# Performance work log

Hardware: AMD Instinct MI355X
Metric: run time of the kernel (lower is better)

Reference implementation:

```python
import jax, jax.numpy as jnp
import numpy as np

N_SRC = 100000
N_DST = 100000
N_EDGES = 300000
FEAT = 256
REV_DIM = 128
REV_VOCAB = 500000


def setup_inputs() -> dict:
    key = jax.random.key(0)
    ks = jax.random.split(key, 14)
    feat = jax.random.normal(ks[0], (N_SRC, FEAT), dtype=jnp.float32)
    cj = jax.random.uniform(ks[1], (N_SRC, 1), dtype=jnp.float32)
    ci = jax.random.uniform(ks[2], (N_DST, 1), dtype=jnp.float32)
    edge_src = jax.random.randint(ks[3], (N_EDGES,), 0, N_SRC)
    edge_dst = jax.random.randint(ks[4], (N_EDGES,), 0, N_DST)
    review_id = jax.random.randint(ks[5], (N_EDGES,), 0, REV_VOCAB)
    s = 0.05
    review_emb = jax.random.normal(ks[6], (REV_VOCAB, REV_DIM), dtype=jnp.float32) * s
    prob_w = jax.random.normal(ks[7], (1, REV_DIM), dtype=jnp.float32) * s      # prob_score
    score_w = jax.random.normal(ks[8], (1, REV_DIM), dtype=jnp.float32) * s     # review_score
    rw1 = jax.random.normal(ks[9], (FEAT, REV_DIM), dtype=jnp.float32) * s      # review_w[0]
    rw2 = jax.random.normal(ks[10], (FEAT, FEAT), dtype=jnp.float32) * s        # review_w[2]
    rw3 = jax.random.normal(ks[11], (FEAT, FEAT), dtype=jnp.float32) * s        # review_w[4]
    lin_w = jax.random.normal(ks[12], (FEAT, FEAT), dtype=jnp.float32) * s      # self.linear
    lin_b = jax.random.normal(ks[13], (FEAT,), dtype=jnp.float32) * s
    return dict(feat=feat, cj=cj, ci=ci, edge_src=edge_src, edge_dst=edge_dst,
                review_id=review_id, review_emb=review_emb, prob_w=prob_w,
                score_w=score_w, rw1=rw1, rw2=rw2, rw3=rw3, lin_w=lin_w, lin_b=lin_b)


def reference(feat, cj, ci, edge_src, edge_dst, review_id,
              review_emb, prob_w, score_w, rw1, rw2, rw3, lin_w, lin_b):
    gelu = lambda x: jax.nn.gelu(x, approximate=False)  # torch default GELU (erf)
    # gather review embeddings per edge: [E, 128]
    rfeat = review_emb[review_id]
    pa = jax.nn.sigmoid(rfeat @ prob_w.T)    # [E, 1]
    ra = jax.nn.sigmoid(rfeat @ score_w.T)   # [E, 1]
    # review_w MLP: 128 -> F -> F -> F, no bias, GELU between
    rf = gelu(gelu(rfeat @ rw1.T) @ rw2.T) @ rw3.T  # [E, F]
    # per-edge message, gated and normalized by src cj (dropout is identity at p=0)
    m = (feat[edge_src] * pa + rf * ra) * cj[edge_src]  # [E, F]
    # scatter-sum to destination nodes
    h = jax.ops.segment_sum(m, edge_dst, num_segments=N_DST)  # [N_dst, F]
    rst = h * ci
    return rst @ lin_w.T + lin_b
```

## Files before the change

### kernel.cpp

```cpp
#include <hip/hip_runtime.h>
#include <math.h>
#include <stdint.h>


typedef short bf16x8 __attribute__((ext_vector_type(8)));
typedef float f32x16 __attribute__((ext_vector_type(16)));

__device__ __forceinline__ float bf2f(unsigned short v) {
    union { unsigned int u; float f; } x; x.u = ((unsigned int)v) << 16; return x.f;
}
__device__ __forceinline__ unsigned short f2bf(float f) {
    union { float f; unsigned int u; } x; x.f = f;
    unsigned int u = x.u;
    return (unsigned short)((u + 0x7FFFu + ((u >> 16) & 1u)) >> 16);
}
__device__ __forceinline__ unsigned pack2(float lo, float hi) {
    unsigned r;
    asm("v_cvt_pk_bf16_f32 %0, %1, %2" : "=v"(r) : "v"(lo), "v"(hi));
    return r;
}
__device__ __forceinline__ float gelu_fast(float x) {
    float y = x * (0.7978845608f + 0.0356774081f * x * x);
    float e = __builtin_amdgcn_exp2f(y * 2.8853900818f);
    float th = 1.0f - 2.0f * __builtin_amdgcn_rcpf(e + 1.0f);
    return 0.5f * x * (1.0f + th);
}
__device__ __forceinline__ float sigmoidf(float x) {
    return 1.0f / (1.0f + expf(-x));
}

__global__ __launch_bounds__(256) void prep_weights(
    const float* __restrict__ rw1, const float* __restrict__ rw2,
    const float* __restrict__ rw3, const float* __restrict__ lw,
    unsigned short* __restrict__ w1s, unsigned short* __restrict__ w2s,
    unsigned short* __restrict__ w3s, unsigned short* __restrict__ lws)
{
    int i = blockIdx.x * blockDim.x + threadIdx.x;
    int j   = i & 7;
    int l   = (i >> 3) & 31;
    int kgg = (i >> 8) & 1;
    int n2  = (i >> 9) & 7;
    int ks  = i >> 12;
    if (i < 32768) {
        w1s[i] = f2bf(rw1[(n2 * 32 + l) * 128 + ks * 16 + kgg * 8 + j]);
    }
    if (i < 65536) {
        int row = n2 * 32 + l, k = ks * 16 + kgg * 8 + j;
        w2s[i] = f2bf(rw2[(size_t)row * 256 + k]);
        w3s[i] = f2bf(rw3[(size_t)row * 256 + k]);
        int ok = (k & 192) | ((k & 1) << 5) | ((k & 63) >> 1);
        lws[i] = f2bf(lw[(size_t)row * 256 + ok]);
    }
}

__device__ __forceinline__ bf16x8 ldw(const unsigned short* __restrict__ W,
                                      int ks, int nglob, int kg, int l31) {
    return *(const bf16x8*)(W + (((((ks * 8 + nglob) * 2) + kg) * 32 + l31) << 3));
}

__global__ __launch_bounds__(256) void hist_kernel(
    const int* __restrict__ edst, int* __restrict__ cnt,
    int* __restrict__ within, int E)
{
    int e = blockIdx.x * blockDim.x + threadIdx.x;
    if (e < E) within[e] = atomicAdd(&cnt[edst[e]], 1);
}

__global__ __launch_bounds__(1024) void scan_block(
    const int* __restrict__ cnt, int* __restrict__ start,
    int* __restrict__ bsum, int n)
{
    __shared__ int s[1024];
    int gid = blockIdx.x * 1024 + threadIdx.x;
    int v = (gid < n) ? cnt[gid] : 0;
    s[threadIdx.x] = v;
    __syncthreads();
    #pragma unroll
    for (int off = 1; off < 1024; off <<= 1) {
        int t = (threadIdx.x >= off) ? s[threadIdx.x - off] : 0;
        __syncthreads();
        if (threadIdx.x >= off) s[threadIdx.x] += t;
        __syncthreads();
    }
    if (gid < n) start[gid] = s[threadIdx.x] - v;
    if (threadIdx.x == 1023) bsum[blockIdx.x] = s[1023];
}

__global__ void scan_bsum(int* __restrict__ bsum, int nb) {
    if (threadIdx.x == 0 && blockIdx.x == 0) {
        int acc = 0;
        for (int i = 0; i < nb; ++i) { int v = bsum[i]; bsum[i] = acc; acc += v; }
    }
}

__global__ __launch_bounds__(1024) void add_offsets(
    int* __restrict__ start, const int* __restrict__ bsum, int n, int E)
{
    int gid = blockIdx.x * 1024 + threadIdx.x;
    if (gid < n) start[gid] += bsum[gid >> 10];
    if (gid == 0) start[n] = E;
}

__global__ __launch_bounds__(256) void build_sorted(
    const int* __restrict__ edst, const int* __restrict__ within,
    const int* __restrict__ start, const int* __restrict__ rid,
    const int* __restrict__ esrc, int* __restrict__ rid_s,
    int* __restrict__ esrc_s, int E)
{
    int e = blockIdx.x * blockDim.x + threadIdx.x;
    if (e < E) {
        int pos = start[edst[e]] + within[e];
        rid_s[pos]  = rid[e];
        esrc_s[pos] = esrc[e];
    }
}

__device__ __forceinline__ bf16x8 ldtf(const unsigned short* t_lds, int row, int ks, int kg) {
    int slot = (ks * 2 + kg) ^ (row & 15);
    return *(const bf16x8*)((const char*)t_lds + row * 512 + slot * 16);
}
__device__ __forceinline__ void sttf(unsigned short* t_lds, int row, int nn, int p, int kg, uint2 w) {
    int slot = (nn * 4 + p) ^ (row & 15);
    *(uint2*)((char*)t_lds + row * 512 + slot * 16 + kg * 8) = w;
}
__device__ __forceinline__ bf16x8 ldrb(const unsigned short* t_rb, int row, int ks, int kg) {
    int slot = (ks * 2 + kg) ^ (row & 15);
    return *(const bf16x8*)((const char*)t_rb + row * 256 + slot * 16);
}

__global__ __launch_bounds__(256, 5) void fused_edge(
    const float* __restrict__ remb, const int* __restrict__ rid_s,
    const int* __restrict__ esrc_s,
    const unsigned short* __restrict__ w1s, const unsigned short* __restrict__ w2s,
    const unsigned short* __restrict__ w3s,
    const float* __restrict__ pw, const float* __restrict__ sw,
    const float* __restrict__ cj, float* __restrict__ ga,
    unsigned short* __restrict__ m, int E)
{
    __shared__ __align__(16) unsigned short t_lds[32 * 256];
    __shared__ __align__(16) unsigned short t_rb[32 * 128];
    __shared__ float gvb_lds[32];

    const int lane = threadIdx.x & 63;
    const int f    = threadIdx.x >> 6;
    const int l31  = lane & 31;
    const int kg   = lane >> 5;
    const int blk0 = blockIdx.x * 32;
    const int i    = blk0 + l31;
    const int ic   = (i < E) ? i : (E - 1);
    const int row_l = l31;

    {
        const int t = threadIdx.x;
        #pragma unroll
        for (int p = 0; p < 2; ++p) {
            int sIdx = p * 256 + t;
            int row  = sIdx >> 4;
            int c16  = sIdx & 15;
            int gr   = blk0 + row;
            int rr   = rid_s[(gr < E) ? gr : (E - 1)];
            const float* sp = remb + (size_t)rr * 128 + c16 * 8;
            float4 a = *(const float4*)sp;
            float4 b = *(const float4*)(sp + 4);
            uint4 w;
            w.x = pack2(a.x, a.y); w.y = pack2(a.z, a.w);
            w.z = pack2(b.x, b.y); w.w = pack2(b.z, b.w);
            int slot = c16 ^ (row & 15);
            *(uint4*)((char*)t_rb + row * 256 + slot * 16) = w;
        }
    }
    __syncthreads();

    {
        f32x16 acc[2];
        acc[0] = (f32x16)0.0f; acc[1] = (f32x16)0.0f;
        float pd = 0.f, rd = 0.f;

        #pragma unroll
        for (int ks = 0; ks < 8; ++ks) {
            bf16x8 af = ldrb(t_rb, row_l, ks, kg);
            if (f == 0) {
                const int kk = ks * 16 + kg * 8;
                float4 p0 = *(const float4*)(pw + kk), p1 = *(const float4*)(pw + kk + 4);
                float4 s0 = *(const float4*)(sw + kk), s1v = *(const float4*)(sw + kk + 4);
                float v0 = bf2f((unsigned short)af[0]), v1 = bf2f((unsigned short)af[1]);
                float v2 = bf2f((unsigned short)af[2]), v3 = bf2f((unsigned short)af[3]);
                float v4 = bf2f((unsigned short)af[4]), v5 = bf2f((unsigned short)af[5]);
                float v6 = bf2f((unsigned short)af[6]), v7 = bf2f((unsigned short)af[7]);
                pd += v0*p0.x + v1*p0.y + v2*p0.z + v3*p0.w
                    + v4*p1.x + v5*p1.y + v6*p1.z + v7*p1.w;
                rd += v0*s0.x + v1*s0.y + v2*s0.z + v3*s0.w
                    + v4*s1v.x + v5*s1v.y + v6*s1v.z + v7*s1v.w;
            }
            #pragma unroll
            for (int n = 0; n < 2; ++n) {
                bf16x8 wf = ldw(w1s, ks, f * 2 + n, kg, l31);
                acc[n] = __builtin_amdgcn_mfma_f32_32x32x16_bf16(wf, af, acc[n], 0, 0, 0);
            }
        }

        if (f == 0) {
            pd += __shfl_xor(pd, 32);
            rd += __shfl_xor(rd, 32);
            if (lane < 32) {
                float cjv = cj[esrc_s[ic]];
                if (i < E) ga[i] = sigmoidf(pd) * cjv;
                gvb_lds[l31] = sigmoidf(rd) * cjv;
            }
        }

        #pragma unroll
        for (int n = 0; n < 2; ++n)
            #pragma unroll
            for (int p = 0; p < 4; ++p) {
                uint2 w;
                w.x = pack2(gelu_fast(acc[n][4*p + 0]), gelu_fast(acc[n][4*p + 1]));
                w.y = pack2(gelu_fast(acc[n][4*p + 2]), gelu_fast(acc[n][4*p + 3]));
                sttf(t_lds, row_l, f * 2 + n, p, kg, w);
            }
    }
    __syncthreads();

    {
        f32x16 acc[2];
        acc[0] = (f32x16)0.0f; acc[1] = (f32x16)0.0f;

        #pragma unroll
        for (int ks = 0; ks < 16; ++ks) {
            bf16x8 tf = ldtf(t_lds, row_l, ks, kg);
            #pragma unroll
            for (int n = 0; n < 2; ++n) {
                bf16x8 wf = ldw(w2s, ks, f * 2 + n, kg, l31);
                acc[n] = __builtin_amdgcn_mfma_f32_32x32x16_bf16(wf, tf, acc[n], 0, 0, 0);
            }
        }
        __syncthreads();
        #pragma unroll
        for (int n = 0; n < 2; ++n)
            #pragma unroll
            for (int p = 0; p < 4; ++p) {
                uint2 w;
                w.x = pack2(gelu_fast(acc[n][4*p + 0]), gelu_fast(acc[n][4*p + 1]));
                w.y = pack2(gelu_fast(acc[n][4*p + 2]), gelu_fast(acc[n][4*p + 3]));
                sttf(t_lds, row_l, f * 2 + n, p, kg, w);
            }
    }
    __syncthreads();

    {
        f32x16 acc[2];
        acc[0] = (f32x16)0.0f; acc[1] = (f32x16)0.0f;

        #pragma unroll
        for (int ks = 0; ks < 16; ++ks) {
            bf16x8 tf = ldtf(t_lds, row_l, ks, kg);
            #pragma unroll
            for (int n = 0; n < 2; ++n) {
                bf16x8 wf = ldw(w3s, ks, f * 2 + n, kg, l31);
                acc[n] = __builtin_amdgcn_mfma_f32_32x32x16_bf16(tf, wf, acc[n], 0, 0, 0);
            }
        }

        #pragma unroll
        for (int r = 0; r < 16; ++r) {
            const int lrow = (r & 3) + 8 * (r >> 2) + 4 * kg;
            const int gi = blk0 + lrow;
            if (gi < E) {
                float gbv = gvb_lds[lrow];
                float v0 = acc[0][r] * gbv;
                float v1 = acc[1][r] * gbv;
                *(unsigned*)(m + (size_t)gi * 256 + f * 64 + l31 * 2) = pack2(v0, v1);
            }
        }
    }
}

__global__ __launch_bounds__(256) void segsum_kernel(
    const int* __restrict__ start, const unsigned short* __restrict__ m,
    const float* __restrict__ ga, const int* __restrict__ esrc_s,
    const float* __restrict__ feat, unsigned short* __restrict__ h, int ND)
{
    int d = blockIdx.x * 4 + (threadIdx.x >> 6);
    if (d >= ND) return;
    int lane = threadIdx.x & 63;
    int q = lane >> 4;
    int b = lane & 15;
    int foff = q * 64 + 2 * b;
    int s0 = start[d], s1 = start[d + 1];
    float a0 = 0.f, a1 = 0.f, a2 = 0.f, a3 = 0.f;
    for (int i = s0; i < s1; ++i) {
        float gav = ga[i];
        const float* fp = feat + (size_t)esrc_s[i] * 256 + foff;
        float2 fa = *(const float2*)fp;
        float2 fb = *(const float2*)(fp + 32);
        ushort4 v = *(const ushort4*)(m + (size_t)i * 256 + lane * 4);
        a0 += bf2f(v.x) + fa.x * gav;
        a1 += bf2f(v.y) + fb.x * gav;
        a2 += bf2f(v.z) + fa.y * gav;
        a3 += bf2f(v.w) + fb.y * gav;
    }
    ushort4 o; o.x = f2bf(a0); o.y = f2bf(a1); o.z = f2bf(a2); o.w = f2bf(a3);
    *(ushort4*)(h + (size_t)d * 256 + lane * 4) = o;
}

__global__ __launch_bounds__(256, 2) void g4_kernel(
    const unsigned short* __restrict__ Ab, const unsigned short* __restrict__ lws,
    float* __restrict__ outf, const float* __restrict__ ci,
    const float* __restrict__ bias, int M)
{
    const int lane = threadIdx.x & 63;
    const int wid  = threadIdx.x >> 6;
    const int l31  = lane & 31;
    const int kg   = lane >> 5;
    const int f    = wid & 1;
    const int wbase = blockIdx.x * 128 + (wid >> 1) * 64;
    const int r0 = wbase + l31, r1 = wbase + 32 + l31;
    const int ar0 = (r0 < M) ? r0 : (M - 1);
    const int ar1 = (r1 < M) ? r1 : (M - 1);

    f32x16 acc[2][4];
    #pragma unroll
    for (int mi = 0; mi < 2; ++mi)
        #pragma unroll
        for (int n = 0; n < 4; ++n) acc[mi][n] = (f32x16)0.0f;

    #pragma unroll
    for (int ks = 0; ks < 16; ++ks) {
        const int kk = ks * 16 + kg * 8;
        bf16x8 a0 = *(const bf16x8*)(Ab + (size_t)ar0 * 256 + kk);
        bf16x8 a1 = *(const bf16x8*)(Ab + (size_t)ar1 * 256 + kk);
        #pragma unroll
        for (int n = 0; n < 4; ++n) {
            bf16x8 b = ldw(lws, ks, f * 4 + n, kg, l31);
            acc[0][n] = __builtin_amdgcn_mfma_f32_32x32x16_bf16(a0, b, acc[0][n], 0, 0, 0);
            acc[1][n] = __builtin_amdgcn_mfma_f32_32x32x16_bf16(a1, b, acc[1][n], 0, 0, 0);
        }
    }
    #pragma unroll
    for (int mi = 0; mi < 2; ++mi) {
        #pragma unroll
        for (int r = 0; r < 16; ++r) {
            const int gr = wbase + mi * 32 + (r & 3) + 8 * (r >> 2) + 4 * kg;
            if (gr >= M) continue;
            float civ = ci[gr];
            #pragma unroll
            for (int n = 0; n < 4; ++n) {
                int col = f * 128 + n * 32 + l31;
                outf[(size_t)gr * 256 + col] = acc[mi][n][r] * civ + bias[col];
            }
        }
    }
}

extern "C" void kernel_launch(void* const* d_in, const int* in_sizes, int n_in,
                              void* d_out, int out_size, void* d_ws, size_t ws_size,
                              hipStream_t stream) {
    const float* feat = (const float*)d_in[0];
    const float* cj   = (const float*)d_in[1];
    const float* ci   = (const float*)d_in[2];
    const int*   esrc = (const int*)d_in[3];
    const int*   edst = (const int*)d_in[4];
    const int*   rid  = (const int*)d_in[5];
    const float* remb = (const float*)d_in[6];
    const float* pw   = (const float*)d_in[7];
    const float* sw   = (const float*)d_in[8];
    const float* rw1  = (const float*)d_in[9];
    const float* rw2  = (const float*)d_in[10];
    const float* rw3  = (const float*)d_in[11];
    const float* lw   = (const float*)d_in[12];
    const float* lb   = (const float*)d_in[13];
    float* out = (float*)d_out;

    const int E  = in_sizes[3];
    const int ND = in_sizes[2];

    char* ws = (char*)d_ws;
    float* ga = (float*)ws;
    unsigned short* m   = (unsigned short*)(ga + E);
    unsigned short* h   = m + (size_t)E * 256;
    unsigned short* w1s = h + (size_t)ND * 256;
    unsigned short* w2s = w1s + 32768;
    unsigned short* w3s = w2s + 65536;
    unsigned short* lws = w3s + 65536;
    int* cnt    = (int*)(lws + 65536);
    int* start  = cnt + ND;
    int* bsum   = start + ND + 1;
    int* within = bsum + 128;
    int* rid_s  = within + E;
    int* esrc_s = rid_s + E;

    const int NB = (ND + 1023) / 1024;

    hipMemsetAsync(cnt, 0, (size_t)ND * sizeof(int), stream);
    prep_weights<<<256, 256, 0, stream>>>(rw1, rw2, rw3, lw, w1s, w2s, w3s, lws);

    hist_kernel<<<(E + 255) / 256, 256, 0, stream>>>(edst, cnt, within, E);
    scan_block<<<NB, 1024, 0, stream>>>(cnt, start, bsum, ND);
    scan_bsum<<<1, 64, 0, stream>>>(bsum, NB);
    add_offsets<<<NB, 1024, 0, stream>>>(start, bsum, ND, E);
    build_sorted<<<(E + 255) / 256, 256, 0, stream>>>(edst, within, start, rid, esrc,
                                                      rid_s, esrc_s, E);

    fused_edge<<<(E + 31) / 32, 256, 0, stream>>>(
        remb, rid_s, esrc_s, w1s, w2s, w3s, pw, sw, cj, ga, m, E);

    segsum_kernel<<<(ND + 3) / 4, 256, 0, stream>>>(start, m, ga, esrc_s, feat, h, ND);

    g4_kernel<<<(ND + 127) / 128, 256, 0, stream>>>(h, lws, out, ci, lb, ND);
}
```

Measured before the change: 418.9 us.

## Fuse segment-sum into edge MLP kernel and drop per-edge message buffer

```diff
diff --git a/kernel.cpp b/kernel.cpp
--- a/kernel.cpp
+++ b/kernel.cpp
@@ -48,8 +48,7 @@
         int row = n2 * 32 + l, k = ks * 16 + kgg * 8 + j;
         w2s[i] = f2bf(rw2[(size_t)row * 256 + k]);
         w3s[i] = f2bf(rw3[(size_t)row * 256 + k]);
-        int ok = (k & 192) | ((k & 1) << 5) | ((k & 63) >> 1);
-        lws[i] = f2bf(lw[(size_t)row * 256 + ok]);
+        lws[i] = f2bf(lw[(size_t)row * 256 + k]);
     }
 }
 
@@ -105,13 +104,15 @@
     const int* __restrict__ edst, const int* __restrict__ within,
     const int* __restrict__ start, const int* __restrict__ rid,
     const int* __restrict__ esrc, int* __restrict__ rid_s,
-    int* __restrict__ esrc_s, int E)
+    int* __restrict__ esrc_s, int* __restrict__ dst_s, int E)
 {
     int e = blockIdx.x * blockDim.x + threadIdx.x;
     if (e < E) {
-        int pos = start[edst[e]] + within[e];
+        int d = edst[e];
+        int pos = start[d] + within[e];
         rid_s[pos]  = rid[e];
         esrc_s[pos] = esrc[e];
+        dst_s[pos]  = d;
     }
 }
 
@@ -130,28 +131,36 @@
 
 __global__ __launch_bounds__(256, 5) void fused_edge(
     const float* __restrict__ remb, const int* __restrict__ rid_s,
-    const int* __restrict__ esrc_s,
+    const int* __restrict__ esrc_s, const int* __restrict__ dst_s,
+    const int* __restrict__ start,
     const unsigned short* __restrict__ w1s, const unsigned short* __restrict__ w2s,
     const unsigned short* __restrict__ w3s,
     const float* __restrict__ pw, const float* __restrict__ sw,
-    const float* __restrict__ cj, float* __restrict__ ga,
-    unsigned short* __restrict__ m, int E)
+    const float* __restrict__ cj, const float* __restrict__ feat,
+    unsigned short* __restrict__ h, int E)
 {
     __shared__ __align__(16) unsigned short t_lds[32 * 256];
     __shared__ __align__(16) unsigned short t_rb[32 * 128];
-    __shared__ float gvb_lds[32];
+    __shared__ float ga_lds[32], gvb_lds[32];
+    __shared__ int dst_lds[32], src_lds[32], cross_lds[32];
 
     const int lane = threadIdx.x & 63;
     const int f    = threadIdx.x >> 6;
     const int l31  = lane & 31;
     const int kg   = lane >> 5;
     const int blk0 = blockIdx.x * 32;
-    const int i    = blk0 + l31;
-    const int ic   = (i < E) ? i : (E - 1);
     const int row_l = l31;
 
     {
         const int t = threadIdx.x;
+        if (t < 32) {
+            int e  = blk0 + t;
+            int ec = (e < E) ? e : (E - 1);
+            int d  = dst_s[ec];
+            dst_lds[t]   = d;
+            src_lds[t]   = esrc_s[ec];
+            cross_lds[t] = (start[d] < blk0) || (start[d + 1] > blk0 + 32);
+        }
         #pragma unroll
         for (int p = 0; p < 2; ++p) {
             int sIdx = p * 256 + t;
@@ -203,8 +212,8 @@
             pd += __shfl_xor(pd, 32);
             rd += __shfl_xor(rd, 32);
             if (lane < 32) {
-                float cjv = cj[esrc_s[ic]];
-                if (i < E) ga[i] = sigmoidf(pd) * cjv;
+                float cjv = cj[src_lds[l31]];
+                ga_lds[l31]  = sigmoidf(pd) * cjv;
                 gvb_lds[l31] = sigmoidf(rd) * cjv;
             }
         }
@@ -262,45 +271,37 @@
         }
 
         #pragma unroll
-        for (int r = 0; r < 16; ++r) {
-            const int lrow = (r & 3) + 8 * (r >> 2) + 4 * kg;
-            const int gi = blk0 + lrow;
-            if (gi < E) {
-                float gbv = gvb_lds[lrow];
-                float v0 = acc[0][r] * gbv;
-                float v1 = acc[1][r] * gbv;
-                *(unsigned*)(m + (size_t)gi * 256 + f * 64 + l31 * 2) = pack2(v0, v1);
-            }
-        }
-    }
-}
-
-__global__ __launch_bounds__(256) void segsum_kernel(
-    const int* __restrict__ start, const unsigned short* __restrict__ m,
-    const float* __restrict__ ga, const int* __restrict__ esrc_s,
-    const float* __restrict__ feat, unsigned short* __restrict__ h, int ND)
-{
-    int d = blockIdx.x * 4 + (threadIdx.x >> 6);
-    if (d >= ND) return;
-    int lane = threadIdx.x & 63;
-    int q = lane >> 4;
-    int b = lane & 15;
-    int foff = q * 64 + 2 * b;
-    int s0 = start[d], s1 = start[d + 1];
-    float a0 = 0.f, a1 = 0.f, a2 = 0.f, a3 = 0.f;
-    for (int i = s0; i < s1; ++i) {
-        float gav = ga[i];
-        const float* fp = feat + (size_t)esrc_s[i] * 256 + foff;
-        float2 fa = *(const float2*)fp;
-        float2 fb = *(const float2*)(fp + 32);
-        ushort4 v = *(const ushort4*)(m + (size_t)i * 256 + lane * 4);
-        a0 += bf2f(v.x) + fa.x * gav;
-        a1 += bf2f(v.y) + fb.x * gav;
-        a2 += bf2f(v.z) + fa.y * gav;
-        a3 += bf2f(v.w) + fb.y * gav;
-    }
-    ushort4 o; o.x = f2bf(a0); o.y = f2bf(a1); o.z = f2bf(a2); o.w = f2bf(a3);
-    *(ushort4*)(h + (size_t)d * 256 + lane * 4) = o;
+        for (int n = 0; n < 2; ++n) {
+            const int col = f * 64 + n * 32 + l31;
+            float sum = 0.f;
+            #pragma unroll
+            for (int e = 0; e < 32; ++e) {
+                if (((e >> 2) & 1) == kg) {
+                    const int r = (e & 3) | ((e >> 3) << 2);
+                    float fv = feat[(size_t)src_lds[e] * 256 + col];
+                    sum += acc[n][r] * gvb_lds[e] + fv * ga_lds[e];
+                }
+                if (e == 31 || dst_lds[e + 1] != dst_lds[e]) {
+                    sum += __shfl_xor(sum, 32);
+                    if (kg == 0) {
+                        int d = dst_lds[e];
+                        unsigned short* hp = h + (size_t)d * 256 + col;
+                        if (!cross_lds[e]) {
+                            *hp = f2bf(sum);
+                        } else {
+                            float oth = __shfl_xor(sum, 1);
+                            if ((l31 & 1) == 0) {
+                                unsigned pk = pack2(sum, oth);
+                                asm volatile("global_atomic_pk_add_bf16 %0, %1, off"
+                                             :: "v"((uint64_t)hp), "v"(pk) : "memory");
+                            }
+                        }
+                    }
+                    sum = 0.f;
+                }
+            }
+        }
+    }
 }
 
 __global__ __launch_bounds__(256, 2) void g4_kernel(
@@ -375,9 +376,7 @@
     const int ND = in_sizes[2];
 
     char* ws = (char*)d_ws;
-    float* ga = (float*)ws;
-    unsigned short* m   = (unsigned short*)(ga + E);
-    unsigned short* h   = m + (size_t)E * 256;
+    unsigned short* h   = (unsigned short*)ws;
     unsigned short* w1s = h + (size_t)ND * 256;
     unsigned short* w2s = w1s + 32768;
     unsigned short* w3s = w2s + 65536;
@@ -388,10 +387,12 @@
     int* within = bsum + 128;
     int* rid_s  = within + E;
     int* esrc_s = rid_s + E;
+    int* dst_s  = esrc_s + E;
 
     const int NB = (ND + 1023) / 1024;
 
     hipMemsetAsync(cnt, 0, (size_t)ND * sizeof(int), stream);
+    hipMemsetAsync(h, 0, (size_t)ND * 256 * sizeof(unsigned short), stream);
     prep_weights<<<256, 256, 0, stream>>>(rw1, rw2, rw3, lw, w1s, w2s, w3s, lws);
 
     hist_kernel<<<(E + 255) / 256, 256, 0, stream>>>(edst, cnt, within, E);
@@ -399,12 +400,10 @@
     scan_bsum<<<1, 64, 0, stream>>>(bsum, NB);
     add_offsets<<<NB, 1024, 0, stream>>>(start, bsum, ND, E);
     build_sorted<<<(E + 255) / 256, 256, 0, stream>>>(edst, within, start, rid, esrc,
-                                                      rid_s, esrc_s, E);
+                                                      rid_s, esrc_s, dst_s, E);
 
     fused_edge<<<(E + 31) / 32, 256, 0, stream>>>(
-        remb, rid_s, esrc_s, w1s, w2s, w3s, pw, sw, cj, ga, m, E);
-
-    segsum_kernel<<<(ND + 3) / 4, 256, 0, stream>>>(start, m, ga, esrc_s, feat, h, ND);
+        remb, rid_s, esrc_s, dst_s, start, w1s, w2s, w3s, pw, sw, cj, feat, h, E);
 
     g4_kernel<<<(ND + 127) / 128, 256, 0, stream>>>(h, lws, out, ci, lb, ND);
 }
```

Result: slower. 560.8 us (+33.9%).

## Fuse segment-sum into final linear GEMM via LDS-staged bf16 tile

Applied to the files above, without the earlier changes.

```diff
diff --git a/kernel.cpp b/kernel.cpp
--- a/kernel.cpp
+++ b/kernel.cpp
@@ -128,7 +128,7 @@
     return *(const bf16x8*)((const char*)t_rb + row * 256 + slot * 16);
 }
 
-__global__ __launch_bounds__(256, 5) void fused_edge(
+__global__ __launch_bounds__(256, 6) void fused_edge(
     const float* __restrict__ remb, const int* __restrict__ rid_s,
     const int* __restrict__ esrc_s,
     const unsigned short* __restrict__ w1s, const unsigned short* __restrict__ w2s,
@@ -275,78 +275,77 @@
     }
 }
 
-__global__ __launch_bounds__(256) void segsum_kernel(
+__global__ __launch_bounds__(256, 4) void g4seg_kernel(
     const int* __restrict__ start, const unsigned short* __restrict__ m,
     const float* __restrict__ ga, const int* __restrict__ esrc_s,
-    const float* __restrict__ feat, unsigned short* __restrict__ h, int ND)
-{
-    int d = blockIdx.x * 4 + (threadIdx.x >> 6);
-    if (d >= ND) return;
-    int lane = threadIdx.x & 63;
-    int q = lane >> 4;
-    int b = lane & 15;
-    int foff = q * 64 + 2 * b;
-    int s0 = start[d], s1 = start[d + 1];
-    float a0 = 0.f, a1 = 0.f, a2 = 0.f, a3 = 0.f;
-    for (int i = s0; i < s1; ++i) {
-        float gav = ga[i];
-        const float* fp = feat + (size_t)esrc_s[i] * 256 + foff;
-        float2 fa = *(const float2*)fp;
-        float2 fb = *(const float2*)(fp + 32);
-        ushort4 v = *(const ushort4*)(m + (size_t)i * 256 + lane * 4);
-        a0 += bf2f(v.x) + fa.x * gav;
-        a1 += bf2f(v.y) + fb.x * gav;
-        a2 += bf2f(v.z) + fa.y * gav;
-        a3 += bf2f(v.w) + fb.y * gav;
-    }
-    ushort4 o; o.x = f2bf(a0); o.y = f2bf(a1); o.z = f2bf(a2); o.w = f2bf(a3);
-    *(ushort4*)(h + (size_t)d * 256 + lane * 4) = o;
-}
-
-__global__ __launch_bounds__(256, 2) void g4_kernel(
-    const unsigned short* __restrict__ Ab, const unsigned short* __restrict__ lws,
+    const float* __restrict__ feat, const unsigned short* __restrict__ lws,
     float* __restrict__ outf, const float* __restrict__ ci,
-    const float* __restrict__ bias, int M)
-{
+    const float* __restrict__ bias, int ND)
+{
+    __shared__ __align__(16) unsigned short h_lds[64 * 256];
+
     const int lane = threadIdx.x & 63;
     const int wid  = threadIdx.x >> 6;
     const int l31  = lane & 31;
     const int kg   = lane >> 5;
-    const int f    = wid & 1;
-    const int wbase = blockIdx.x * 128 + (wid >> 1) * 64;
-    const int r0 = wbase + l31, r1 = wbase + 32 + l31;
-    const int ar0 = (r0 < M) ? r0 : (M - 1);
-    const int ar1 = (r1 < M) ? r1 : (M - 1);
-
-    f32x16 acc[2][4];
-    #pragma unroll
-    for (int mi = 0; mi < 2; ++mi)
-        #pragma unroll
-        for (int n = 0; n < 4; ++n) acc[mi][n] = (f32x16)0.0f;
-
-    #pragma unroll
-    for (int ks = 0; ks < 16; ++ks) {
-        const int kk = ks * 16 + kg * 8;
-        bf16x8 a0 = *(const bf16x8*)(Ab + (size_t)ar0 * 256 + kk);
-        bf16x8 a1 = *(const bf16x8*)(Ab + (size_t)ar1 * 256 + kk);
-        #pragma unroll
-        for (int n = 0; n < 4; ++n) {
-            bf16x8 b = ldw(lws, ks, f * 4 + n, kg, l31);
-            acc[0][n] = __builtin_amdgcn_mfma_f32_32x32x16_bf16(a0, b, acc[0][n], 0, 0, 0);
-            acc[1][n] = __builtin_amdgcn_mfma_f32_32x32x16_bf16(a1, b, acc[1][n], 0, 0, 0);
-        }
-    }
-    #pragma unroll
-    for (int mi = 0; mi < 2; ++mi) {
+    const int d0   = blockIdx.x * 64;
+
+    {
+        int q = lane >> 4;
+        int b = lane & 15;
+        int foff = q * 64 + 2 * b;
+        for (int j = 0; j < 16; ++j) {
+            int dl = wid * 16 + j;
+            int d  = d0 + dl;
+            float a0 = 0.f, a1 = 0.f, a2 = 0.f, a3 = 0.f;
+            if (d < ND) {
+                int s0 = start[d], s1 = start[d + 1];
+                for (int i = s0; i < s1; ++i) {
+                    float gav = ga[i];
+                    const float* fp = feat + (size_t)esrc_s[i] * 256 + foff;
+                    float2 fa = *(const float2*)fp;
+                    float2 fb = *(const float2*)(fp + 32);
+                    ushort4 v = *(const ushort4*)(m + (size_t)i * 256 + lane * 4);
+                    a0 += bf2f(v.x) + fa.x * gav;
+                    a1 += bf2f(v.y) + fb.x * gav;
+                    a2 += bf2f(v.z) + fa.y * gav;
+                    a3 += bf2f(v.w) + fb.y * gav;
+                }
+            }
+            uint2 w; w.x = pack2(a0, a1); w.y = pack2(a2, a3);
+            int slot = (lane >> 1) ^ (dl & 15);
+            *(uint2*)((char*)h_lds + dl * 512 + slot * 16 + (lane & 1) * 8) = w;
+        }
+    }
+    __syncthreads();
+
+    {
+        const int rg = wid >> 1;
+        const int fh = wid & 1;
+        const int arow = rg * 32 + l31;
+
+        f32x16 acc[4];
+        #pragma unroll
+        for (int n = 0; n < 4; ++n) acc[n] = (f32x16)0.0f;
+
+        #pragma unroll
+        for (int ks = 0; ks < 16; ++ks) {
+            bf16x8 a0 = ldtf(h_lds, arow, ks, kg);
+            #pragma unroll
+            for (int n = 0; n < 4; ++n) {
+                bf16x8 b = ldw(lws, ks, fh * 4 + n, kg, l31);
+                acc[n] = __builtin_amdgcn_mfma_f32_32x32x16_bf16(a0, b, acc[n], 0, 0, 0);
+            }
+        }
         #pragma unroll
         for (int r = 0; r < 16; ++r) {
-            const int gr = wbase + mi * 32 + (r & 3) + 8 * (r >> 2) + 4 * kg;
-            if (gr >= M) continue;
+            const int gr = d0 + rg * 32 + (r & 3) + 8 * (r >> 2) + 4 * kg;
+            if (gr >= ND) continue;
             float civ = ci[gr];
             #pragma unroll
             for (int n = 0; n < 4; ++n) {
-                int col = f * 128 + n * 32 + l31;
-                outf[(size_t)gr * 256 + col] = acc[mi][n][r] * civ + bias[col];
+                int col = fh * 128 + n * 32 + l31;
+                outf[(size_t)gr * 256 + col] = acc[n][r] * civ + bias[col];
             }
         }
     }
@@ -377,8 +376,7 @@
     char* ws = (char*)d_ws;
     float* ga = (float*)ws;
     unsigned short* m   = (unsigned short*)(ga + E);
-    unsigned short* h   = m + (size_t)E * 256;
-    unsigned short* w1s = h + (size_t)ND * 256;
+    unsigned short* w1s = m + (size_t)E * 256;
     unsigned short* w2s = w1s + 32768;
     unsigned short* w3s = w2s + 65536;
     unsigned short* lws = w3s + 65536;
@@ -404,7 +402,6 @@
     fused_edge<<<(E + 31) / 32, 256, 0, stream>>>(
         remb, rid_s, esrc_s, w1s, w2s, w3s, pw, sw, cj, ga, m, E);
 
-    segsum_kernel<<<(ND + 3) / 4, 256, 0, stream>>>(start, m, ga, esrc_s, feat, h, ND);
-
-    g4_kernel<<<(ND + 127) / 128, 256, 0, stream>>>(h, lws, out, ci, lb, ND);
-}
+    g4seg_kernel<<<(ND + 63) / 64, 256, 0, stream>>>(
+        start, m, ga, esrc_s, feat, lws, out, ci, lb, ND);
+}
```

Result: slower. 486.9 us (+16.2%).
